# Kernel optimization log

Measured on AMD Instinct MI355X. Metric: run time of the kernel, lower is better.

## Reference

```python
import jax, jax.numpy as jnp
import numpy as np

N_NODES = 100000
N_EDGES = 800000
D_IN = 256
D_HID = 256
D_OUT = 64


def _gcn_conv(x, W, b, src, dst, deg_inv_sqrt, n_nodes):
    """PyG GCNConv: out = D^{-1/2}(A+I)D^{-1/2} (x @ W) + b.
    src/dst already include self-loops; deg_inv_sqrt precomputed over them."""
    h = x @ W  # [N, Dh]
    norm = deg_inv_sqrt[src] * deg_inv_sqrt[dst]  # [E+N]
    msg = h[src] * norm[:, None]  # gather + scale, [E+N, Dh]
    out = jax.ops.segment_sum(msg, dst, num_segments=n_nodes)  # scatter-add
    return out + b


def setup_inputs() -> dict:
    key = jax.random.key(0)
    ks = jax.random.split(key, 8)
    x = jax.random.normal(ks[0], (N_NODES, D_IN), jnp.float32)
    edge_index = jax.random.randint(ks[1], (2, N_EDGES), 0, N_NODES, dtype=jnp.int32)
    W1 = jax.random.normal(ks[2], (D_IN, D_HID), jnp.float32) * (1.0 / np.sqrt(D_IN))
    b1 = jnp.zeros((D_HID,), jnp.float32)
    W2 = jax.random.normal(ks[3], (D_HID, D_HID), jnp.float32) * (1.0 / np.sqrt(D_HID))
    b2 = jnp.zeros((D_HID,), jnp.float32)
    Wo = jax.random.normal(ks[4], (D_HID, D_OUT), jnp.float32) * (1.0 / np.sqrt(D_HID))
    bo = jnp.zeros((D_OUT,), jnp.float32)
    return {"x": x, "edge_index": edge_index, "W1": W1, "b1": b1,
            "W2": W2, "b2": b2, "Wo": Wo, "bo": bo}


def reference(x, edge_index, W1, b1, W2, b2, Wo, bo):
    n = x.shape[0]
    loops = jnp.arange(n, dtype=edge_index.dtype)
    src = jnp.concatenate([edge_index[0], loops])  # add self-loops
    dst = jnp.concatenate([edge_index[1], loops])
    # degree over target nodes (incl. self-loops), symmetric normalization
    deg = jax.ops.segment_sum(jnp.ones(dst.shape[0], x.dtype), dst, num_segments=n)
    deg_inv_sqrt = jax.lax.rsqrt(deg)  # deg >= 1 thanks to self-loops

    h = _gcn_conv(x, W1, b1, src, dst, deg_inv_sqrt, n)
    h = jax.nn.relu(h)
    # dropout p=0.0 -> identity
    h = _gcn_conv(h, W2, b2, src, dst, deg_inv_sqrt, n)
    h = jax.nn.relu(h)
    logits = h @ Wo + bo
    return jax.nn.log_softmax(logits, axis=1)
```

## Files before the change

### kernel.cpp

```cpp
#include <hip/hip_runtime.h>
#include <math.h>

#define TPB 256

typedef short bf16x8 __attribute__((ext_vector_type(8)));
typedef unsigned short u16x8 __attribute__((ext_vector_type(8)));
typedef float f32x4 __attribute__((ext_vector_type(4)));

__device__ __forceinline__ float bf2f(unsigned short u) {
  union { unsigned int i; float f; } c;
  c.i = ((unsigned int)u) << 16;
  return c.f;
}
__device__ __forceinline__ unsigned short f2bf(float f) {
  union { float f; unsigned int i; } c;
  c.f = f;
  unsigned int r = c.i + 0x7FFFu + ((c.i >> 16) & 1u);
  return (unsigned short)(r >> 16);
}


__global__ __launch_bounds__(TPB) void zero_cnt_k(int* __restrict__ cnt, int N) {
  int i = blockIdx.x * TPB + threadIdx.x;
  if (i < N) cnt[i] = 0;
}

__global__ __launch_bounds__(TPB) void count_k(const int* __restrict__ dstv,
                                               int* __restrict__ cnt, int E) {
  int e = blockIdx.x * TPB + threadIdx.x;
  if (e < E) atomicAdd(&cnt[dstv[e]], 1);
}

__global__ __launch_bounds__(TPB) void scan1_k(const int* __restrict__ cnt,
                                               int* __restrict__ excl,
                                               int* __restrict__ blk_sums, int N) {
  __shared__ int sh[TPB];
  int b = blockIdx.x, tid = threadIdx.x;
  int base = b * 1024 + tid * 4;
  int v[4];
  int sum = 0;
#pragma unroll
  for (int j = 0; j < 4; ++j) {
    int i = base + j;
    v[j] = (i < N) ? cnt[i] : 0;
    sum += v[j];
  }
  sh[tid] = sum;
  __syncthreads();
  for (int off = 1; off < TPB; off <<= 1) {
    int t = (tid >= off) ? sh[tid - off] : 0;
    __syncthreads();
    sh[tid] += t;
    __syncthreads();
  }
  if (tid == TPB - 1) blk_sums[b] = sh[TPB - 1];
  int run = (tid > 0) ? sh[tid - 1] : 0;
#pragma unroll
  for (int j = 0; j < 4; ++j) {
    int i = base + j;
    if (i < N) excl[i] = run;
    run += v[j];
  }
}

__global__ __launch_bounds__(TPB) void scan2_k(int* __restrict__ blk_sums, int NB) {
  __shared__ int sh[TPB];
  int tid = threadIdx.x;
  sh[tid] = (tid < NB) ? blk_sums[tid] : 0;
  __syncthreads();
  for (int off = 1; off < TPB; off <<= 1) {
    int t = (tid >= off) ? sh[tid - off] : 0;
    __syncthreads();
    sh[tid] += t;
    __syncthreads();
  }
  int ex = (tid > 0) ? sh[tid - 1] : 0;
  if (tid < NB) blk_sums[tid] = ex;
}

__global__ __launch_bounds__(TPB) void finalize_k(int* __restrict__ row_ptr,
                                                  const int* __restrict__ blk_sums,
                                                  int* __restrict__ cursor,
                                                  const int* __restrict__ cnt,
                                                  float* __restrict__ dis, int N, int E) {
  int i = blockIdx.x * TPB + threadIdx.x;
  if (i < N) {
    int r = row_ptr[i] + blk_sums[i >> 10];
    row_ptr[i] = r;
    cursor[i] = r;
    dis[i] = rsqrtf((float)(cnt[i] + 1));
  }
  if (blockIdx.x == 0 && threadIdx.x == 0) row_ptr[N] = E;
}

__global__ __launch_bounds__(TPB) void fill_k(const int* __restrict__ srcv,
                                              const int* __restrict__ dstv,
                                              int* __restrict__ cursor,
                                              int* __restrict__ col_src, int E) {
  int e = blockIdx.x * TPB + threadIdx.x;
  if (e < E) {
    int d = dstv[e];
    int pos = atomicAdd(&cursor[d], 1);
    col_src[pos] = srcv[e];
  }
}


__global__ __launch_bounds__(TPB) void cvt_bf16_k(const float* __restrict__ in,
                                                  unsigned short* __restrict__ out,
                                                  long n) {
  long i = ((long)blockIdx.x * TPB + threadIdx.x) * 8;
  if (i >= n) return;
  float4 a = *(const float4*)(in + i);
  float4 b = *(const float4*)(in + i + 4);
  ushort4 o0, o1;
  o0.x = f2bf(a.x); o0.y = f2bf(a.y); o0.z = f2bf(a.z); o0.w = f2bf(a.w);
  o1.x = f2bf(b.x); o1.y = f2bf(b.y); o1.z = f2bf(b.z); o1.w = f2bf(b.w);
  *(ushort4*)(out + i) = o0;
  *(ushort4*)(out + i + 4) = o1;
}

__global__ __launch_bounds__(TPB) void wt_k(const float* __restrict__ W,
                                            unsigned short* __restrict__ Wt) {
  int idx = blockIdx.x * TPB + threadIdx.x;
  int n = idx >> 8, k = idx & 255;
  Wt[n * 256 + k] = f2bf(W[k * 256 + n]);
}

__global__ __launch_bounds__(TPB) void wot_k(const float* __restrict__ Wo,
                                             unsigned short* __restrict__ Wot) {
  int idx = blockIdx.x * TPB + threadIdx.x;
  int n = idx >> 8, k = idx & 255;
  Wot[n * 256 + k] = f2bf(Wo[k * 64 + n]);
}


__global__ __launch_bounds__(TPB) void gemm_bf16_k(const unsigned short* __restrict__ A,
                                                   const unsigned short* __restrict__ Bt,
                                                   unsigned short* __restrict__ C,
                                                   const float* __restrict__ dis,
                                                   int M) {
  __shared__ unsigned short As[128 * 32];
  __shared__ unsigned short Bs[128 * 32];
  const int tid = threadIdx.x;
  const int m0 = blockIdx.y * 128;
  const int n0 = blockIdx.x * 128;
  const int lane = tid & 63;
  const int wid = tid >> 6;
  const int wr = (wid >> 1) * 64;
  const int wc = (wid & 1) * 64;

  const int srow = tid >> 1;
  const int scb0 = (tid & 1) * 2;
  const int grow = min(m0 + srow, M - 1);
  const unsigned short* gA = A + (size_t)grow * 256 + scb0 * 8;
  const unsigned short* gB = Bt + (size_t)(n0 + srow) * 256 + scb0 * 8;
  const int swz = (srow >> 1) & 3;
  const int ls0 = srow * 64 + ((scb0 ^ swz) << 4);
  const int ls1 = srow * 64 + (((scb0 + 1) ^ swz) << 4);

  const int r15 = lane & 15;
  const int cq = lane >> 4;
  const int swzr = (r15 >> 1) & 3;
  const int coff = ((cq ^ swzr) << 4);

  f32x4 acc[4][4];
#pragma unroll
  for (int i = 0; i < 4; ++i)
#pragma unroll
    for (int j = 0; j < 4; ++j)
#pragma unroll
      for (int r = 0; r < 4; ++r) acc[i][j][r] = 0.f;

  u16x8 ra0 = *(const u16x8*)(gA);
  u16x8 ra1 = *(const u16x8*)(gA + 8);
  u16x8 rb0 = *(const u16x8*)(gB);
  u16x8 rb1 = *(const u16x8*)(gB + 8);

  for (int kt = 0; kt < 8; ++kt) {
    __syncthreads();
    *(u16x8*)((char*)As + ls0) = ra0;
    *(u16x8*)((char*)As + ls1) = ra1;
    *(u16x8*)((char*)Bs + ls0) = rb0;
    *(u16x8*)((char*)Bs + ls1) = rb1;
    __syncthreads();
    if (kt < 7) {
      ra0 = *(const u16x8*)(gA + (kt + 1) * 32);
      ra1 = *(const u16x8*)(gA + (kt + 1) * 32 + 8);
      rb0 = *(const u16x8*)(gB + (kt + 1) * 32);
      rb1 = *(const u16x8*)(gB + (kt + 1) * 32 + 8);
    }
    bf16x8 af[4], bfr[4];
#pragma unroll
    for (int i = 0; i < 4; ++i)
      af[i] = *(const bf16x8*)((char*)As + (wr + i * 16 + r15) * 64 + coff);
#pragma unroll
    for (int j = 0; j < 4; ++j)
      bfr[j] = *(const bf16x8*)((char*)Bs + (wc + j * 16 + r15) * 64 + coff);
#pragma unroll
    for (int i = 0; i < 4; ++i)
#pragma unroll
      for (int j = 0; j < 4; ++j)
        acc[i][j] = __builtin_amdgcn_mfma_f32_16x16x32_bf16(af[i], bfr[j], acc[i][j], 0, 0, 0);
  }

#pragma unroll
  for (int i = 0; i < 4; ++i) {
#pragma unroll
    for (int r = 0; r < 4; ++r) {
      int row = m0 + wr + i * 16 + (lane >> 4) * 4 + r;
      if (row < M) {
        float dv = dis[row];
#pragma unroll
        for (int j = 0; j < 4; ++j) {
          C[(size_t)row * 256 + n0 + wc + j * 16 + r15] = f2bf(dv * acc[i][j][r]);
        }
      }
    }
  }
}


__global__ __launch_bounds__(TPB) void aggregate_bf_k(const unsigned short* __restrict__ H,
                                                      unsigned short* __restrict__ O,
                                                      const int* __restrict__ row_ptr,
                                                      const int* __restrict__ col_src,
                                                      const float* __restrict__ dis,
                                                      const float* __restrict__ bias,
                                                      int N) {
  int wid = (blockIdx.x * TPB + threadIdx.x) >> 6;
  int lane = threadIdx.x & 63;
  if (wid >= N) return;
  int beg = row_ptr[wid], end = row_ptr[wid + 1];

  float p0 = 0.f, p1 = 0.f, p2 = 0.f, p3 = 0.f;
  float q0 = 0.f, q1 = 0.f, q2 = 0.f, q3 = 0.f;
  float r0 = 0.f, r1 = 0.f, r2 = 0.f, r3 = 0.f;
  float t0 = 0.f, t1 = 0.f, t2 = 0.f, t3 = 0.f;

  int e = beg;
  for (; e + 4 <= end; e += 4) {
    int s0 = col_src[e + 0];
    int s1 = col_src[e + 1];
    int s2 = col_src[e + 2];
    int s3 = col_src[e + 3];
    ushort4 h0 = *(const ushort4*)(H + (size_t)s0 * 256 + lane * 4);
    ushort4 h1 = *(const ushort4*)(H + (size_t)s1 * 256 + lane * 4);
    ushort4 h2 = *(const ushort4*)(H + (size_t)s2 * 256 + lane * 4);
    ushort4 h3 = *(const ushort4*)(H + (size_t)s3 * 256 + lane * 4);
    p0 += bf2f(h0.x); p1 += bf2f(h0.y); p2 += bf2f(h0.z); p3 += bf2f(h0.w);
    q0 += bf2f(h1.x); q1 += bf2f(h1.y); q2 += bf2f(h1.z); q3 += bf2f(h1.w);
    r0 += bf2f(h2.x); r1 += bf2f(h2.y); r2 += bf2f(h2.z); r3 += bf2f(h2.w);
    t0 += bf2f(h3.x); t1 += bf2f(h3.y); t2 += bf2f(h3.z); t3 += bf2f(h3.w);
  }
  for (; e < end; ++e) {
    int s = col_src[e];
    ushort4 h = *(const ushort4*)(H + (size_t)s * 256 + lane * 4);
    p0 += bf2f(h.x); p1 += bf2f(h.y); p2 += bf2f(h.z); p3 += bf2f(h.w);
  }

  ushort4 hv = *(const ushort4*)(H + (size_t)wid * 256 + lane * 4);
  p0 += bf2f(hv.x); p1 += bf2f(hv.y); p2 += bf2f(hv.z); p3 += bf2f(hv.w);

  float s0 = (p0 + q0) + (r0 + t0);
  float s1 = (p1 + q1) + (r1 + t1);
  float s2 = (p2 + q2) + (r2 + t2);
  float s3 = (p3 + q3) + (r3 + t3);

  float dv = dis[wid];
  float4 b = *(const float4*)(bias + lane * 4);
  ushort4 o;
  o.x = f2bf(fmaxf(fmaf(dv, s0, b.x), 0.f));
  o.y = f2bf(fmaxf(fmaf(dv, s1, b.y), 0.f));
  o.z = f2bf(fmaxf(fmaf(dv, s2, b.z), 0.f));
  o.w = f2bf(fmaxf(fmaf(dv, s3, b.w), 0.f));
  *(ushort4*)(O + (size_t)wid * 256 + lane * 4) = o;
}


__global__ __launch_bounds__(TPB) void outgemm_k(const unsigned short* __restrict__ H,
                                                 const unsigned short* __restrict__ Wot,
                                                 const float* __restrict__ bo,
                                                 float* __restrict__ out, int M) {
  __shared__ unsigned short As[128 * 32];
  __shared__ unsigned short Bs[64 * 32];
  __shared__ float Ls[128][65];
  const int tid = threadIdx.x;
  const int m0 = blockIdx.x * 128;
  const int lane = tid & 63;
  const int w = tid >> 6;
  const int wr = w * 32;

  const int srow = tid >> 1;
  const int scb0 = (tid & 1) * 2;
  const int grow = min(m0 + srow, M - 1);
  const unsigned short* gA = H + (size_t)grow * 256 + scb0 * 8;
  const int swz = (srow >> 1) & 3;
  const int lsa0 = srow * 64 + ((scb0 ^ swz) << 4);
  const int lsa1 = srow * 64 + (((scb0 + 1) ^ swz) << 4);

  const int brow = tid >> 2;
  const int bcb = tid & 3;
  const unsigned short* gB = Wot + (size_t)brow * 256 + bcb * 8;
  const int bswz = (brow >> 1) & 3;
  const int lsb = brow * 64 + ((bcb ^ bswz) << 4);

  const int r15 = lane & 15;
  const int cq = lane >> 4;
  const int swzr = (r15 >> 1) & 3;
  const int coff = ((cq ^ swzr) << 4);

  f32x4 acc[2][4];
#pragma unroll
  for (int i = 0; i < 2; ++i)
#pragma unroll
    for (int j = 0; j < 4; ++j)
#pragma unroll
      for (int r = 0; r < 4; ++r) acc[i][j][r] = 0.f;

  u16x8 ra0 = *(const u16x8*)(gA);
  u16x8 ra1 = *(const u16x8*)(gA + 8);
  u16x8 rb = *(const u16x8*)(gB);

  for (int kt = 0; kt < 8; ++kt) {
    __syncthreads();
    *(u16x8*)((char*)As + lsa0) = ra0;
    *(u16x8*)((char*)As + lsa1) = ra1;
    *(u16x8*)((char*)Bs + lsb) = rb;
    __syncthreads();
    if (kt < 7) {
      ra0 = *(const u16x8*)(gA + (kt + 1) * 32);
      ra1 = *(const u16x8*)(gA + (kt + 1) * 32 + 8);
      rb = *(const u16x8*)(gB + (kt + 1) * 32);
    }
    bf16x8 af[2], bfr[4];
#pragma unroll
    for (int i = 0; i < 2; ++i)
      af[i] = *(const bf16x8*)((char*)As + (wr + i * 16 + r15) * 64 + coff);
#pragma unroll
    for (int j = 0; j < 4; ++j)
      bfr[j] = *(const bf16x8*)((char*)Bs + (j * 16 + r15) * 64 + coff);
#pragma unroll
    for (int i = 0; i < 2; ++i)
#pragma unroll
      for (int j = 0; j < 4; ++j)
        acc[i][j] = __builtin_amdgcn_mfma_f32_16x16x32_bf16(af[i], bfr[j], acc[i][j], 0, 0, 0);
  }

#pragma unroll
  for (int j = 0; j < 4; ++j) {
    float bj = bo[j * 16 + r15];
#pragma unroll
    for (int i = 0; i < 2; ++i)
#pragma unroll
      for (int r = 0; r < 4; ++r) {
        int rl = wr + i * 16 + (lane >> 4) * 4 + r;
        Ls[rl][j * 16 + r15] = acc[i][j][r] + bj;
      }
  }
  __syncthreads();

  for (int r = wr; r < wr + 32; ++r) {
    int gr = m0 + r;
    if (gr >= M) break;
    float v = Ls[r][lane];
    float mx = v;
    for (int o = 32; o > 0; o >>= 1) mx = fmaxf(mx, __shfl_xor(mx, o, 64));
    float ex = expf(v - mx);
    float s = ex;
    for (int o = 32; o > 0; o >>= 1) s += __shfl_xor(s, o, 64);
    out[(size_t)gr * 64 + lane] = (v - mx) - logf(s);
  }
}


extern "C" void kernel_launch(void* const* d_in, const int* in_sizes, int n_in,
                              void* d_out, int out_size, void* d_ws, size_t ws_size,
                              hipStream_t stream) {
  const float* x = (const float*)d_in[0];
  const int* ei = (const int*)d_in[1];
  const float* W1 = (const float*)d_in[2];
  const float* b1 = (const float*)d_in[3];
  const float* W2 = (const float*)d_in[4];
  const float* b2 = (const float*)d_in[5];
  const float* Wo = (const float*)d_in[6];
  const float* bo = (const float*)d_in[7];
  float* out = (float*)d_out;

  const int Dh = 256;
  const int N = in_sizes[0] / Dh;
  const int E = in_sizes[1] / 2;
  const int* srcv = ei;
  const int* dstv = ei + E;

  char* p = (char*)d_ws;
  auto take = [&](size_t bytes) {
    char* r = p;
    p += (bytes + 255) & ~(size_t)255;
    return r;
  };
  unsigned short* xbf = (unsigned short*)take((size_t)N * Dh * 2);
  unsigned short* hbuf1 = (unsigned short*)take((size_t)N * Dh * 2);
  unsigned short* hbuf2 = (unsigned short*)take((size_t)N * Dh * 2);
  unsigned short* Wt1 = (unsigned short*)take(256 * 256 * 2);
  unsigned short* Wt2 = (unsigned short*)take(256 * 256 * 2);
  unsigned short* Wot = (unsigned short*)take(64 * 256 * 2);
  float* dis = (float*)take((size_t)N * 4);
  int* cnt = (int*)take((size_t)N * 4);
  int* row_ptr = (int*)take((size_t)(N + 1) * 4);
  int* cursor = (int*)take((size_t)N * 4);
  int* col_src = (int*)take((size_t)E * 4);
  int* blk_sums = (int*)take(4096 * 4);

  int NB = (N + 1023) / 1024;

  long nx = (long)N * Dh;
  cvt_bf16_k<<<(int)((nx / 8 + TPB - 1) / TPB), TPB, 0, stream>>>(x, xbf, nx);
  wt_k<<<256, TPB, 0, stream>>>(W1, Wt1);
  wt_k<<<256, TPB, 0, stream>>>(W2, Wt2);
  wot_k<<<64, TPB, 0, stream>>>(Wo, Wot);
  zero_cnt_k<<<(N + TPB - 1) / TPB, TPB, 0, stream>>>(cnt, N);
  count_k<<<(E + TPB - 1) / TPB, TPB, 0, stream>>>(dstv, cnt, E);
  scan1_k<<<NB, TPB, 0, stream>>>(cnt, row_ptr, blk_sums, N);
  scan2_k<<<1, TPB, 0, stream>>>(blk_sums, NB);
  finalize_k<<<(N + TPB - 1) / TPB, TPB, 0, stream>>>(row_ptr, blk_sums, cursor, cnt, dis, N, E);
  fill_k<<<(E + TPB - 1) / TPB, TPB, 0, stream>>>(srcv, dstv, cursor, col_src, E);

  dim3 ggrid(2, (N + 127) / 128);

  gemm_bf16_k<<<ggrid, TPB, 0, stream>>>(xbf, Wt1, hbuf1, dis, N);
  aggregate_bf_k<<<(N + 3) / 4, TPB, 0, stream>>>(hbuf1, hbuf2, row_ptr, col_src, dis, b1, N);
  gemm_bf16_k<<<ggrid, TPB, 0, stream>>>(hbuf2, Wt2, hbuf1, dis, N);
  aggregate_bf_k<<<(N + 3) / 4, TPB, 0, stream>>>(hbuf1, hbuf2, row_ptr, col_src, dis, b2, N);
  outgemm_k<<<(N + 127) / 128, TPB, 0, stream>>>(hbuf2, Wot, bo, out, N);
}
```

Before: 530.0 us.

## Fuse fp32-to-bf16 conversion into first GEMM and widen aggregation gathers

Removes the separate conversion kernel and its bf16 copy of x. The first GEMM now reads fp32 x directly and packs it to bf16 in registers, which saves a full write and re-read of a 51MB buffer, though each A-tile load in that GEMM now moves twice the bytes. The aggregation kernel now has each half-wave handle a different edge with 16-byte loads, so more gathers are in flight per wave. The two halves are combined with a cross-lane shuffle, and one extra row load is used to pad the odd-edge tail.

```diff
diff --git a/kernel.cpp b/kernel.cpp
--- a/kernel.cpp
+++ b/kernel.cpp
@@ -17,6 +17,12 @@
   c.f = f;
   unsigned int r = c.i + 0x7FFFu + ((c.i >> 16) & 1u);
   return (unsigned short)(r >> 16);
+}
+__device__ __forceinline__ u16x8 pack8(float4 a, float4 b) {
+  u16x8 r;
+  r[0] = f2bf(a.x); r[1] = f2bf(a.y); r[2] = f2bf(a.z); r[3] = f2bf(a.w);
+  r[4] = f2bf(b.x); r[5] = f2bf(b.y); r[6] = f2bf(b.z); r[7] = f2bf(b.w);
+  return r;
 }
 
 
@@ -106,20 +112,6 @@
 }
 
 
-__global__ __launch_bounds__(TPB) void cvt_bf16_k(const float* __restrict__ in,
-                                                  unsigned short* __restrict__ out,
-                                                  long n) {
-  long i = ((long)blockIdx.x * TPB + threadIdx.x) * 8;
-  if (i >= n) return;
-  float4 a = *(const float4*)(in + i);
-  float4 b = *(const float4*)(in + i + 4);
-  ushort4 o0, o1;
-  o0.x = f2bf(a.x); o0.y = f2bf(a.y); o0.z = f2bf(a.z); o0.w = f2bf(a.w);
-  o1.x = f2bf(b.x); o1.y = f2bf(b.y); o1.z = f2bf(b.z); o1.w = f2bf(b.w);
-  *(ushort4*)(out + i) = o0;
-  *(ushort4*)(out + i + 4) = o1;
-}
-
 __global__ __launch_bounds__(TPB) void wt_k(const float* __restrict__ W,
                                             unsigned short* __restrict__ Wt) {
   int idx = blockIdx.x * TPB + threadIdx.x;
@@ -135,7 +127,8 @@
 }
 
 
-__global__ __launch_bounds__(TPB) void gemm_bf16_k(const unsigned short* __restrict__ A,
+template <bool AF32>
+__global__ __launch_bounds__(TPB) void gemm_bf16_t(const void* __restrict__ Araw,
                                                    const unsigned short* __restrict__ Bt,
                                                    unsigned short* __restrict__ C,
                                                    const float* __restrict__ dis,
@@ -153,7 +146,8 @@
   const int srow = tid >> 1;
   const int scb0 = (tid & 1) * 2;
   const int grow = min(m0 + srow, M - 1);
-  const unsigned short* gA = A + (size_t)grow * 256 + scb0 * 8;
+  const float* gA32 = (const float*)Araw + (size_t)grow * 256 + scb0 * 8;
+  const unsigned short* gA16 = (const unsigned short*)Araw + (size_t)grow * 256 + scb0 * 8;
   const unsigned short* gB = Bt + (size_t)(n0 + srow) * 256 + scb0 * 8;
   const int swz = (srow >> 1) & 3;
   const int ls0 = srow * 64 + ((scb0 ^ swz) << 4);
@@ -172,8 +166,18 @@
 #pragma unroll
       for (int r = 0; r < 4; ++r) acc[i][j][r] = 0.f;
 
-  u16x8 ra0 = *(const u16x8*)(gA);
-  u16x8 ra1 = *(const u16x8*)(gA + 8);
+  u16x8 ra0, ra1;
+  if constexpr (AF32) {
+    float4 f0 = *(const float4*)(gA32);
+    float4 f1 = *(const float4*)(gA32 + 4);
+    float4 f2 = *(const float4*)(gA32 + 8);
+    float4 f3 = *(const float4*)(gA32 + 12);
+    ra0 = pack8(f0, f1);
+    ra1 = pack8(f2, f3);
+  } else {
+    ra0 = *(const u16x8*)(gA16);
+    ra1 = *(const u16x8*)(gA16 + 8);
+  }
   u16x8 rb0 = *(const u16x8*)(gB);
   u16x8 rb1 = *(const u16x8*)(gB + 8);
 
@@ -185,8 +189,17 @@
     *(u16x8*)((char*)Bs + ls1) = rb1;
     __syncthreads();
     if (kt < 7) {
-      ra0 = *(const u16x8*)(gA + (kt + 1) * 32);
-      ra1 = *(const u16x8*)(gA + (kt + 1) * 32 + 8);
+      if constexpr (AF32) {
+        float4 f0 = *(const float4*)(gA32 + (kt + 1) * 32);
+        float4 f1 = *(const float4*)(gA32 + (kt + 1) * 32 + 4);
+        float4 f2 = *(const float4*)(gA32 + (kt + 1) * 32 + 8);
+        float4 f3 = *(const float4*)(gA32 + (kt + 1) * 32 + 12);
+        ra0 = pack8(f0, f1);
+        ra1 = pack8(f2, f3);
+      } else {
+        ra0 = *(const u16x8*)(gA16 + (kt + 1) * 32);
+        ra1 = *(const u16x8*)(gA16 + (kt + 1) * 32 + 8);
+      }
       rb0 = *(const u16x8*)(gB + (kt + 1) * 32);
       rb1 = *(const u16x8*)(gB + (kt + 1) * 32 + 8);
     }
@@ -231,50 +244,61 @@
   int wid = (blockIdx.x * TPB + threadIdx.x) >> 6;
   int lane = threadIdx.x & 63;
   if (wid >= N) return;
+  const int half = lane >> 5;
+  const int l5 = lane & 31;
+  const size_t co = (size_t)l5 * 8;
   int beg = row_ptr[wid], end = row_ptr[wid + 1];
 
-  float p0 = 0.f, p1 = 0.f, p2 = 0.f, p3 = 0.f;
-  float q0 = 0.f, q1 = 0.f, q2 = 0.f, q3 = 0.f;
-  float r0 = 0.f, r1 = 0.f, r2 = 0.f, r3 = 0.f;
-  float t0 = 0.f, t1 = 0.f, t2 = 0.f, t3 = 0.f;
+  float a0[8], a1[8], a2[8], a3[8];
+#pragma unroll
+  for (int j = 0; j < 8; ++j) { a0[j] = 0.f; a1[j] = 0.f; a2[j] = 0.f; a3[j] = 0.f; }
 
   int e = beg;
-  for (; e + 4 <= end; e += 4) {
-    int s0 = col_src[e + 0];
-    int s1 = col_src[e + 1];
-    int s2 = col_src[e + 2];
-    int s3 = col_src[e + 3];
-    ushort4 h0 = *(const ushort4*)(H + (size_t)s0 * 256 + lane * 4);
-    ushort4 h1 = *(const ushort4*)(H + (size_t)s1 * 256 + lane * 4);
-    ushort4 h2 = *(const ushort4*)(H + (size_t)s2 * 256 + lane * 4);
-    ushort4 h3 = *(const ushort4*)(H + (size_t)s3 * 256 + lane * 4);
-    p0 += bf2f(h0.x); p1 += bf2f(h0.y); p2 += bf2f(h0.z); p3 += bf2f(h0.w);
-    q0 += bf2f(h1.x); q1 += bf2f(h1.y); q2 += bf2f(h1.z); q3 += bf2f(h1.w);
-    r0 += bf2f(h2.x); r1 += bf2f(h2.y); r2 += bf2f(h2.z); r3 += bf2f(h2.w);
-    t0 += bf2f(h3.x); t1 += bf2f(h3.y); t2 += bf2f(h3.z); t3 += bf2f(h3.w);
-  }
-  for (; e < end; ++e) {
-    int s = col_src[e];
-    ushort4 h = *(const ushort4*)(H + (size_t)s * 256 + lane * 4);
-    p0 += bf2f(h.x); p1 += bf2f(h.y); p2 += bf2f(h.z); p3 += bf2f(h.w);
-  }
-
-  ushort4 hv = *(const ushort4*)(H + (size_t)wid * 256 + lane * 4);
-  p0 += bf2f(hv.x); p1 += bf2f(hv.y); p2 += bf2f(hv.z); p3 += bf2f(hv.w);
-
-  float s0 = (p0 + q0) + (r0 + t0);
-  float s1 = (p1 + q1) + (r1 + t1);
-  float s2 = (p2 + q2) + (r2 + t2);
-  float s3 = (p3 + q3) + (r3 + t3);
+  for (; e + 8 <= end; e += 8) {
+    int s0 = col_src[e + 0 + half];
+    int s1 = col_src[e + 2 + half];
+    int s2 = col_src[e + 4 + half];
+    int s3 = col_src[e + 6 + half];
+    u16x8 h0 = *(const u16x8*)(H + (size_t)s0 * 256 + co);
+    u16x8 h1 = *(const u16x8*)(H + (size_t)s1 * 256 + co);
+    u16x8 h2 = *(const u16x8*)(H + (size_t)s2 * 256 + co);
+    u16x8 h3 = *(const u16x8*)(H + (size_t)s3 * 256 + co);
+#pragma unroll
+    for (int j = 0; j < 8; ++j) {
+      a0[j] += bf2f(h0[j]);
+      a1[j] += bf2f(h1[j]);
+      a2[j] += bf2f(h2[j]);
+      a3[j] += bf2f(h3[j]);
+    }
+  }
+  for (; e < end; e += 2) {
+    int idx = e + half;
+    int ok = idx < end;
+    int s = ok ? col_src[idx] : wid;
+    u16x8 h = *(const u16x8*)(H + (size_t)s * 256 + co);
+    float m = ok ? 1.f : 0.f;
+#pragma unroll
+    for (int j = 0; j < 8; ++j) a0[j] = fmaf(m, bf2f(h[j]), a0[j]);
+  }
+
+  float s[8];
+#pragma unroll
+  for (int j = 0; j < 8; ++j) s[j] = (a0[j] + a1[j]) + (a2[j] + a3[j]);
+#pragma unroll
+  for (int j = 0; j < 8; ++j) s[j] += __shfl_xor(s[j], 32, 64);
+
+  u16x8 hv = *(const u16x8*)(H + (size_t)wid * 256 + co);
+#pragma unroll
+  for (int j = 0; j < 8; ++j) s[j] += bf2f(hv[j]);
 
   float dv = dis[wid];
-  float4 b = *(const float4*)(bias + lane * 4);
-  ushort4 o;
-  o.x = f2bf(fmaxf(fmaf(dv, s0, b.x), 0.f));
-  o.y = f2bf(fmaxf(fmaf(dv, s1, b.y), 0.f));
-  o.z = f2bf(fmaxf(fmaf(dv, s2, b.z), 0.f));
-  o.w = f2bf(fmaxf(fmaf(dv, s3, b.w), 0.f));
-  *(ushort4*)(O + (size_t)wid * 256 + lane * 4) = o;
+  float4 b0 = *(const float4*)(bias + l5 * 8);
+  float4 b1 = *(const float4*)(bias + l5 * 8 + 4);
+  float bb[8] = {b0.x, b0.y, b0.z, b0.w, b1.x, b1.y, b1.z, b1.w};
+  u16x8 o;
+#pragma unroll
+  for (int j = 0; j < 8; ++j) o[j] = f2bf(fmaxf(fmaf(dv, s[j], bb[j]), 0.f));
+  if (half == 0) *(u16x8*)(O + (size_t)wid * 256 + co) = o;
 }
 
 
@@ -367,9 +391,9 @@
     float mx = v;
     for (int o = 32; o > 0; o >>= 1) mx = fmaxf(mx, __shfl_xor(mx, o, 64));
     float ex = expf(v - mx);
-    float s = ex;
-    for (int o = 32; o > 0; o >>= 1) s += __shfl_xor(s, o, 64);
-    out[(size_t)gr * 64 + lane] = (v - mx) - logf(s);
+    float sm = ex;
+    for (int o = 32; o > 0; o >>= 1) sm += __shfl_xor(sm, o, 64);
+    out[(size_t)gr * 64 + lane] = (v - mx) - logf(sm);
   }
 }
 
@@ -399,7 +423,6 @@
     p += (bytes + 255) & ~(size_t)255;
     return r;
   };
-  unsigned short* xbf = (unsigned short*)take((size_t)N * Dh * 2);
   unsigned short* hbuf1 = (unsigned short*)take((size_t)N * Dh * 2);
   unsigned short* hbuf2 = (unsigned short*)take((size_t)N * Dh * 2);
   unsigned short* Wt1 = (unsigned short*)take(256 * 256 * 2);
@@ -414,8 +437,6 @@
 
   int NB = (N + 1023) / 1024;
 
-  long nx = (long)N * Dh;
-  cvt_bf16_k<<<(int)((nx / 8 + TPB - 1) / TPB), TPB, 0, stream>>>(x, xbf, nx);
   wt_k<<<256, TPB, 0, stream>>>(W1, Wt1);
   wt_k<<<256, TPB, 0, stream>>>(W2, Wt2);
   wot_k<<<64, TPB, 0, stream>>>(Wo, Wot);
@@ -428,9 +449,9 @@
 
   dim3 ggrid(2, (N + 127) / 128);
 
-  gemm_bf16_k<<<ggrid, TPB, 0, stream>>>(xbf, Wt1, hbuf1, dis, N);
+  gemm_bf16_t<true><<<ggrid, TPB, 0, stream>>>((const void*)x, Wt1, hbuf1, dis, N);
   aggregate_bf_k<<<(N + 3) / 4, TPB, 0, stream>>>(hbuf1, hbuf2, row_ptr, col_src, dis, b1, N);
-  gemm_bf16_k<<<ggrid, TPB, 0, stream>>>(hbuf2, Wt2, hbuf1, dis, N);
+  gemm_bf16_t<false><<<ggrid, TPB, 0, stream>>>((const void*)hbuf2, Wt2, hbuf1, dis, N);
   aggregate_bf_k<<<(N + 3) / 4, TPB, 0, stream>>>(hbuf1, hbuf2, row_ptr, col_src, dis, b2, N);
   outgemm_k<<<(N + 127) / 128, TPB, 0, stream>>>(hbuf2, Wot, bo, out, N);
 }
```

Result: no change. 520.1 us (-1.9%).

## Fuse fp32-to-bf16 input conversion into first GEMM, double-buffer LDS, XCD-aware block mapping

Applied to the files above, without the earlier changes.

Removes the separate kernel that converted x to bf16. The first GEMM now reads fp32 x directly and packs it to bf16 in registers, which saves writing and re-reading a 51MB intermediate. The GEMM also double-buffers its shared-memory tiles, dropping one barrier per k-step. It remaps a 1D grid so the two N-halves of the same row block land on the same XCD, for L2 reuse of A. The cost is more register pressure and twice the LDS use, which may lower occupancy.

```diff
diff --git a/kernel.cpp b/kernel.cpp
--- a/kernel.cpp
+++ b/kernel.cpp
@@ -17,6 +17,12 @@
   c.f = f;
   unsigned int r = c.i + 0x7FFFu + ((c.i >> 16) & 1u);
   return (unsigned short)(r >> 16);
+}
+__device__ __forceinline__ u16x8 pack8(float4 a, float4 b) {
+  u16x8 r;
+  r[0] = f2bf(a.x); r[1] = f2bf(a.y); r[2] = f2bf(a.z); r[3] = f2bf(a.w);
+  r[4] = f2bf(b.x); r[5] = f2bf(b.y); r[6] = f2bf(b.z); r[7] = f2bf(b.w);
+  return r;
 }
 
 
@@ -106,20 +112,6 @@
 }
 
 
-__global__ __launch_bounds__(TPB) void cvt_bf16_k(const float* __restrict__ in,
-                                                  unsigned short* __restrict__ out,
-                                                  long n) {
-  long i = ((long)blockIdx.x * TPB + threadIdx.x) * 8;
-  if (i >= n) return;
-  float4 a = *(const float4*)(in + i);
-  float4 b = *(const float4*)(in + i + 4);
-  ushort4 o0, o1;
-  o0.x = f2bf(a.x); o0.y = f2bf(a.y); o0.z = f2bf(a.z); o0.w = f2bf(a.w);
-  o1.x = f2bf(b.x); o1.y = f2bf(b.y); o1.z = f2bf(b.z); o1.w = f2bf(b.w);
-  *(ushort4*)(out + i) = o0;
-  *(ushort4*)(out + i + 4) = o1;
-}
-
 __global__ __launch_bounds__(TPB) void wt_k(const float* __restrict__ W,
                                             unsigned short* __restrict__ Wt) {
   int idx = blockIdx.x * TPB + threadIdx.x;
@@ -135,16 +127,24 @@
 }
 
 
-__global__ __launch_bounds__(TPB) void gemm_bf16_k(const unsigned short* __restrict__ A,
+template <bool AF32>
+__global__ __launch_bounds__(TPB) void gemm_bf16_t(const void* __restrict__ Araw,
                                                    const unsigned short* __restrict__ Bt,
                                                    unsigned short* __restrict__ C,
                                                    const float* __restrict__ dis,
-                                                   int M) {
-  __shared__ unsigned short As[128 * 32];
-  __shared__ unsigned short Bs[128 * 32];
+                                                   int M, int nyb) {
+  __shared__ unsigned short As[2][128 * 32];
+  __shared__ unsigned short Bs[2][128 * 32];
+  const int bid = blockIdx.x;
+  const int xcd = bid & 7;
+  const int s = bid >> 3;
+  const int nsel = s & 1;
+  const int yb = (s >> 1) * 8 + xcd;
+  if (yb >= nyb) return;
+  const int m0 = yb * 128;
+  const int n0 = nsel * 128;
+
   const int tid = threadIdx.x;
-  const int m0 = blockIdx.y * 128;
-  const int n0 = blockIdx.x * 128;
   const int lane = tid & 63;
   const int wid = tid >> 6;
   const int wr = (wid >> 1) * 64;
@@ -153,7 +153,8 @@
   const int srow = tid >> 1;
   const int scb0 = (tid & 1) * 2;
   const int grow = min(m0 + srow, M - 1);
-  const unsigned short* gA = A + (size_t)grow * 256 + scb0 * 8;
+  const float* gA32 = (const float*)Araw + (size_t)grow * 256 + scb0 * 8;
+  const unsigned short* gA16 = (const unsigned short*)Araw + (size_t)grow * 256 + scb0 * 8;
   const unsigned short* gB = Bt + (size_t)(n0 + srow) * 256 + scb0 * 8;
   const int swz = (srow >> 1) & 3;
   const int ls0 = srow * 64 + ((scb0 ^ swz) << 4);
@@ -172,31 +173,50 @@
 #pragma unroll
       for (int r = 0; r < 4; ++r) acc[i][j][r] = 0.f;
 
-  u16x8 ra0 = *(const u16x8*)(gA);
-  u16x8 ra1 = *(const u16x8*)(gA + 8);
+  u16x8 ra0, ra1;
+  if constexpr (AF32) {
+    float4 f0 = *(const float4*)(gA32);
+    float4 f1 = *(const float4*)(gA32 + 4);
+    float4 f2 = *(const float4*)(gA32 + 8);
+    float4 f3 = *(const float4*)(gA32 + 12);
+    ra0 = pack8(f0, f1);
+    ra1 = pack8(f2, f3);
+  } else {
+    ra0 = *(const u16x8*)(gA16);
+    ra1 = *(const u16x8*)(gA16 + 8);
+  }
   u16x8 rb0 = *(const u16x8*)(gB);
   u16x8 rb1 = *(const u16x8*)(gB + 8);
 
   for (int kt = 0; kt < 8; ++kt) {
-    __syncthreads();
-    *(u16x8*)((char*)As + ls0) = ra0;
-    *(u16x8*)((char*)As + ls1) = ra1;
-    *(u16x8*)((char*)Bs + ls0) = rb0;
-    *(u16x8*)((char*)Bs + ls1) = rb1;
+    const int cur = kt & 1;
+    *(u16x8*)((char*)As[cur] + ls0) = ra0;
+    *(u16x8*)((char*)As[cur] + ls1) = ra1;
+    *(u16x8*)((char*)Bs[cur] + ls0) = rb0;
+    *(u16x8*)((char*)Bs[cur] + ls1) = rb1;
     __syncthreads();
     if (kt < 7) {
-      ra0 = *(const u16x8*)(gA + (kt + 1) * 32);
-      ra1 = *(const u16x8*)(gA + (kt + 1) * 32 + 8);
+      if constexpr (AF32) {
+        float4 f0 = *(const float4*)(gA32 + (kt + 1) * 32);
+        float4 f1 = *(const float4*)(gA32 + (kt + 1) * 32 + 4);
+        float4 f2 = *(const float4*)(gA32 + (kt + 1) * 32 + 8);
+        float4 f3 = *(const float4*)(gA32 + (kt + 1) * 32 + 12);
+        ra0 = pack8(f0, f1);
+        ra1 = pack8(f2, f3);
+      } else {
+        ra0 = *(const u16x8*)(gA16 + (kt + 1) * 32);
+        ra1 = *(const u16x8*)(gA16 + (kt + 1) * 32 + 8);
+      }
       rb0 = *(const u16x8*)(gB + (kt + 1) * 32);
       rb1 = *(const u16x8*)(gB + (kt + 1) * 32 + 8);
     }
     bf16x8 af[4], bfr[4];
 #pragma unroll
     for (int i = 0; i < 4; ++i)
-      af[i] = *(const bf16x8*)((char*)As + (wr + i * 16 + r15) * 64 + coff);
+      af[i] = *(const bf16x8*)((char*)As[cur] + (wr + i * 16 + r15) * 64 + coff);
 #pragma unroll
     for (int j = 0; j < 4; ++j)
-      bfr[j] = *(const bf16x8*)((char*)Bs + (wc + j * 16 + r15) * 64 + coff);
+      bfr[j] = *(const bf16x8*)((char*)Bs[cur] + (wc + j * 16 + r15) * 64 + coff);
 #pragma unroll
     for (int i = 0; i < 4; ++i)
 #pragma unroll
@@ -367,9 +387,9 @@
     float mx = v;
     for (int o = 32; o > 0; o >>= 1) mx = fmaxf(mx, __shfl_xor(mx, o, 64));
     float ex = expf(v - mx);
-    float s = ex;
-    for (int o = 32; o > 0; o >>= 1) s += __shfl_xor(s, o, 64);
-    out[(size_t)gr * 64 + lane] = (v - mx) - logf(s);
+    float sm = ex;
+    for (int o = 32; o > 0; o >>= 1) sm += __shfl_xor(sm, o, 64);
+    out[(size_t)gr * 64 + lane] = (v - mx) - logf(sm);
   }
 }
 
@@ -399,7 +419,6 @@
     p += (bytes + 255) & ~(size_t)255;
     return r;
   };
-  unsigned short* xbf = (unsigned short*)take((size_t)N * Dh * 2);
   unsigned short* hbuf1 = (unsigned short*)take((size_t)N * Dh * 2);
   unsigned short* hbuf2 = (unsigned short*)take((size_t)N * Dh * 2);
   unsigned short* Wt1 = (unsigned short*)take(256 * 256 * 2);
@@ -414,8 +433,6 @@
 
   int NB = (N + 1023) / 1024;
 
-  long nx = (long)N * Dh;
-  cvt_bf16_k<<<(int)((nx / 8 + TPB - 1) / TPB), TPB, 0, stream>>>(x, xbf, nx);
   wt_k<<<256, TPB, 0, stream>>>(W1, Wt1);
   wt_k<<<256, TPB, 0, stream>>>(W2, Wt2);
   wot_k<<<64, TPB, 0, stream>>>(Wo, Wot);
@@ -426,11 +443,12 @@
   finalize_k<<<(N + TPB - 1) / TPB, TPB, 0, stream>>>(row_ptr, blk_sums, cursor, cnt, dis, N, E);
   fill_k<<<(E + TPB - 1) / TPB, TPB, 0, stream>>>(srcv, dstv, cursor, col_src, E);
 
-  dim3 ggrid(2, (N + 127) / 128);
-
-  gemm_bf16_k<<<ggrid, TPB, 0, stream>>>(xbf, Wt1, hbuf1, dis, N);
+  const int nyb = (N + 127) / 128;
+  const int gblocks = 8 * 2 * ((nyb + 7) / 8);
+
+  gemm_bf16_t<true><<<gblocks, TPB, 0, stream>>>((const void*)x, Wt1, hbuf1, dis, N, nyb);
   aggregate_bf_k<<<(N + 3) / 4, TPB, 0, stream>>>(hbuf1, hbuf2, row_ptr, col_src, dis, b1, N);
-  gemm_bf16_k<<<ggrid, TPB, 0, stream>>>(hbuf2, Wt2, hbuf1, dis, N);
+  gemm_bf16_t<false><<<gblocks, TPB, 0, stream>>>((const void*)hbuf2, Wt2, hbuf1, dis, N, nyb);
   aggregate_bf_k<<<(N + 3) / 4, TPB, 0, stream>>>(hbuf1, hbuf2, row_ptr, col_src, dis, b2, N);
   outgemm_k<<<(N + 127) / 128, TPB, 0, stream>>>(hbuf2, Wot, bo, out, N);
 }
```

New measurement: 508.2 us. -4.1%, faster.

## Stream row tiles against resident LDS weights and fuse input bf16 conversion

Applied to the files above, without the earlier changes.

The GEMMs become persistent kernels that load the full 256x256 bf16 weight into LDS once per block. Each wave then streams 16-row tiles of A straight from global memory into registers. The first-layer GEMM converts the fp32 input to bf16 on the fly, which removes the separate conversion kernel and its intermediate buffer. The output GEMM keeps logits in registers and does log-softmax with 16-lane shuffles instead of staging them through LDS. This trades the tiled A reuse of the old kernel for fewer syncs, 128KB of LDS per block, and register-heavy 16-accumulator tiles, which may limit occupancy.

```diff
diff --git a/kernel.cpp b/kernel.cpp
--- a/kernel.cpp
+++ b/kernel.cpp
@@ -106,20 +106,6 @@
 }
 
 
-__global__ __launch_bounds__(TPB) void cvt_bf16_k(const float* __restrict__ in,
-                                                  unsigned short* __restrict__ out,
-                                                  long n) {
-  long i = ((long)blockIdx.x * TPB + threadIdx.x) * 8;
-  if (i >= n) return;
-  float4 a = *(const float4*)(in + i);
-  float4 b = *(const float4*)(in + i + 4);
-  ushort4 o0, o1;
-  o0.x = f2bf(a.x); o0.y = f2bf(a.y); o0.z = f2bf(a.z); o0.w = f2bf(a.w);
-  o1.x = f2bf(b.x); o1.y = f2bf(b.y); o1.z = f2bf(b.z); o1.w = f2bf(b.w);
-  *(ushort4*)(out + i) = o0;
-  *(ushort4*)(out + i + 4) = o1;
-}
-
 __global__ __launch_bounds__(TPB) void wt_k(const float* __restrict__ W,
                                             unsigned short* __restrict__ Wt) {
   int idx = blockIdx.x * TPB + threadIdx.x;
@@ -135,86 +121,86 @@
 }
 
 
-__global__ __launch_bounds__(TPB) void gemm_bf16_k(const unsigned short* __restrict__ A,
-                                                   const unsigned short* __restrict__ Bt,
-                                                   unsigned short* __restrict__ C,
-                                                   const float* __restrict__ dis,
-                                                   int M) {
-  __shared__ unsigned short As[128 * 32];
-  __shared__ unsigned short Bs[128 * 32];
+template <bool AF32>
+__global__ __launch_bounds__(1024) void gemm_stream_t(const void* __restrict__ Araw,
+                                                      const unsigned short* __restrict__ Bt,
+                                                      unsigned short* __restrict__ C,
+                                                      const float* __restrict__ dis,
+                                                      int M, int ntiles) {
+  __shared__ unsigned short Bs[256 * 256];
   const int tid = threadIdx.x;
-  const int m0 = blockIdx.y * 128;
-  const int n0 = blockIdx.x * 128;
+
+  {
+    const int n = tid >> 2;
+    const int sb = tid & 3;
+    const unsigned short* src = Bt + (size_t)n * 256;
+#pragma unroll
+    for (int it = 0; it < 8; ++it) {
+      int s = sb + 4 * it;
+      u16x8 v = *(const u16x8*)(src + s * 8);
+      *(u16x8*)((char*)Bs + n * 512 + ((s ^ (n & 7)) << 4)) = v;
+    }
+  }
+  __syncthreads();
+
   const int lane = tid & 63;
-  const int wid = tid >> 6;
-  const int wr = (wid >> 1) * 64;
-  const int wc = (wid & 1) * 64;
-
-  const int srow = tid >> 1;
-  const int scb0 = (tid & 1) * 2;
-  const int grow = min(m0 + srow, M - 1);
-  const unsigned short* gA = A + (size_t)grow * 256 + scb0 * 8;
-  const unsigned short* gB = Bt + (size_t)(n0 + srow) * 256 + scb0 * 8;
-  const int swz = (srow >> 1) & 3;
-  const int ls0 = srow * 64 + ((scb0 ^ swz) << 4);
-  const int ls1 = srow * 64 + (((scb0 + 1) ^ swz) << 4);
-
   const int r15 = lane & 15;
   const int cq = lane >> 4;
-  const int swzr = (r15 >> 1) & 3;
-  const int coff = ((cq ^ swzr) << 4);
-
-  f32x4 acc[4][4];
-#pragma unroll
-  for (int i = 0; i < 4; ++i)
-#pragma unroll
-    for (int j = 0; j < 4; ++j)
-#pragma unroll
-      for (int r = 0; r < 4; ++r) acc[i][j][r] = 0.f;
-
-  u16x8 ra0 = *(const u16x8*)(gA);
-  u16x8 ra1 = *(const u16x8*)(gA + 8);
-  u16x8 rb0 = *(const u16x8*)(gB);
-  u16x8 rb1 = *(const u16x8*)(gB + 8);
-
-  for (int kt = 0; kt < 8; ++kt) {
-    __syncthreads();
-    *(u16x8*)((char*)As + ls0) = ra0;
-    *(u16x8*)((char*)As + ls1) = ra1;
-    *(u16x8*)((char*)Bs + ls0) = rb0;
-    *(u16x8*)((char*)Bs + ls1) = rb1;
-    __syncthreads();
-    if (kt < 7) {
-      ra0 = *(const u16x8*)(gA + (kt + 1) * 32);
-      ra1 = *(const u16x8*)(gA + (kt + 1) * 32 + 8);
-      rb0 = *(const u16x8*)(gB + (kt + 1) * 32);
-      rb1 = *(const u16x8*)(gB + (kt + 1) * 32 + 8);
-    }
-    bf16x8 af[4], bfr[4];
-#pragma unroll
-    for (int i = 0; i < 4; ++i)
-      af[i] = *(const bf16x8*)((char*)As + (wr + i * 16 + r15) * 64 + coff);
-#pragma unroll
-    for (int j = 0; j < 4; ++j)
-      bfr[j] = *(const bf16x8*)((char*)Bs + (wc + j * 16 + r15) * 64 + coff);
-#pragma unroll
-    for (int i = 0; i < 4; ++i)
-#pragma unroll
-      for (int j = 0; j < 4; ++j)
-        acc[i][j] = __builtin_amdgcn_mfma_f32_16x16x32_bf16(af[i], bfr[j], acc[i][j], 0, 0, 0);
-  }
-
-#pragma unroll
-  for (int i = 0; i < 4; ++i) {
+  const int gw = blockIdx.x * 16 + (tid >> 6);
+  const int nw = gridDim.x * 16;
+
+  for (int mt = gw; mt < ntiles; mt += nw) {
+    const int m0 = mt * 16;
+    const int arow = min(m0 + r15, M - 1);
+
+    bf16x8 a[8];
+    if constexpr (AF32) {
+      const float* ap = (const float*)Araw + (size_t)arow * 256 + cq * 8;
+#pragma unroll
+      for (int kt = 0; kt < 8; ++kt) {
+        float4 f0 = *(const float4*)(ap + kt * 32);
+        float4 f1 = *(const float4*)(ap + kt * 32 + 4);
+        u16x8 t;
+        t[0] = f2bf(f0.x); t[1] = f2bf(f0.y); t[2] = f2bf(f0.z); t[3] = f2bf(f0.w);
+        t[4] = f2bf(f1.x); t[5] = f2bf(f1.y); t[6] = f2bf(f1.z); t[7] = f2bf(f1.w);
+        a[kt] = (bf16x8)t;
+      }
+    } else {
+      const unsigned short* ap = (const unsigned short*)Araw + (size_t)arow * 256 + cq * 8;
+#pragma unroll
+      for (int kt = 0; kt < 8; ++kt) a[kt] = *(const bf16x8*)(ap + kt * 32);
+    }
+
+    f32x4 acc[16];
+#pragma unroll
+    for (int j = 0; j < 16; ++j)
+#pragma unroll
+      for (int r = 0; r < 4; ++r) acc[j][r] = 0.f;
+
+#pragma unroll
+    for (int kt = 0; kt < 8; ++kt) {
+#pragma unroll
+      for (int j = 0; j < 16; ++j) {
+        int n = j * 16 + r15;
+        int s = kt * 4 + cq;
+        bf16x8 b = *(const bf16x8*)((char*)Bs + n * 512 + ((s ^ (n & 7)) << 4));
+        acc[j] = __builtin_amdgcn_mfma_f32_16x16x32_bf16(a[kt], b, acc[j], 0, 0, 0);
+      }
+    }
+
+    float dv[4];
 #pragma unroll
     for (int r = 0; r < 4; ++r) {
-      int row = m0 + wr + i * 16 + (lane >> 4) * 4 + r;
+      int row = m0 + cq * 4 + r;
+      dv[r] = (row < M) ? dis[row] : 0.f;
+    }
+#pragma unroll
+    for (int r = 0; r < 4; ++r) {
+      int row = m0 + cq * 4 + r;
       if (row < M) {
-        float dv = dis[row];
-#pragma unroll
-        for (int j = 0; j < 4; ++j) {
-          C[(size_t)row * 256 + n0 + wc + j * 16 + r15] = f2bf(dv * acc[i][j][r]);
-        }
+        unsigned short* cp = C + (size_t)row * 256 + r15;
+#pragma unroll
+        for (int j = 0; j < 16; ++j) cp[j * 16] = f2bf(dv[r] * acc[j][r]);
       }
     }
   }
@@ -278,98 +264,82 @@
 }
 
 
-__global__ __launch_bounds__(TPB) void outgemm_k(const unsigned short* __restrict__ H,
-                                                 const unsigned short* __restrict__ Wot,
-                                                 const float* __restrict__ bo,
-                                                 float* __restrict__ out, int M) {
-  __shared__ unsigned short As[128 * 32];
-  __shared__ unsigned short Bs[64 * 32];
-  __shared__ float Ls[128][65];
+__global__ __launch_bounds__(512) void outgemm_stream_k(const unsigned short* __restrict__ H,
+                                                        const unsigned short* __restrict__ Wot,
+                                                        const float* __restrict__ bo,
+                                                        float* __restrict__ out,
+                                                        int M, int ntiles) {
+  __shared__ unsigned short Bs[64 * 256];
   const int tid = threadIdx.x;
-  const int m0 = blockIdx.x * 128;
+
+  {
+    const int n = tid >> 3;
+    const int sb = tid & 7;
+    const unsigned short* src = Wot + (size_t)n * 256;
+#pragma unroll
+    for (int it = 0; it < 4; ++it) {
+      int s = sb + 8 * it;
+      u16x8 v = *(const u16x8*)(src + s * 8);
+      *(u16x8*)((char*)Bs + n * 512 + ((s ^ (n & 7)) << 4)) = v;
+    }
+  }
+  __syncthreads();
+
   const int lane = tid & 63;
-  const int w = tid >> 6;
-  const int wr = w * 32;
-
-  const int srow = tid >> 1;
-  const int scb0 = (tid & 1) * 2;
-  const int grow = min(m0 + srow, M - 1);
-  const unsigned short* gA = H + (size_t)grow * 256 + scb0 * 8;
-  const int swz = (srow >> 1) & 3;
-  const int lsa0 = srow * 64 + ((scb0 ^ swz) << 4);
-  const int lsa1 = srow * 64 + (((scb0 + 1) ^ swz) << 4);
-
-  const int brow = tid >> 2;
-  const int bcb = tid & 3;
-  const unsigned short* gB = Wot + (size_t)brow * 256 + bcb * 8;
-  const int bswz = (brow >> 1) & 3;
-  const int lsb = brow * 64 + ((bcb ^ bswz) << 4);
-
   const int r15 = lane & 15;
   const int cq = lane >> 4;
-  const int swzr = (r15 >> 1) & 3;
-  const int coff = ((cq ^ swzr) << 4);
-
-  f32x4 acc[2][4];
-#pragma unroll
-  for (int i = 0; i < 2; ++i)
-#pragma unroll
-    for (int j = 0; j < 4; ++j)
-#pragma unroll
-      for (int r = 0; r < 4; ++r) acc[i][j][r] = 0.f;
-
-  u16x8 ra0 = *(const u16x8*)(gA);
-  u16x8 ra1 = *(const u16x8*)(gA + 8);
-  u16x8 rb = *(const u16x8*)(gB);
-
+  const int mt = blockIdx.x * 8 + (tid >> 6);
+  if (mt >= ntiles) return;
+  const int m0 = mt * 16;
+  const int arow = min(m0 + r15, M - 1);
+
+  bf16x8 a[8];
+  {
+    const unsigned short* ap = H + (size_t)arow * 256 + cq * 8;
+#pragma unroll
+    for (int kt = 0; kt < 8; ++kt) a[kt] = *(const bf16x8*)(ap + kt * 32);
+  }
+
+  f32x4 acc[4];
+#pragma unroll
+  for (int j = 0; j < 4; ++j)
+#pragma unroll
+    for (int r = 0; r < 4; ++r) acc[j][r] = 0.f;
+
+#pragma unroll
   for (int kt = 0; kt < 8; ++kt) {
-    __syncthreads();
-    *(u16x8*)((char*)As + lsa0) = ra0;
-    *(u16x8*)((char*)As + lsa1) = ra1;
-    *(u16x8*)((char*)Bs + lsb) = rb;
-    __syncthreads();
-    if (kt < 7) {
-      ra0 = *(const u16x8*)(gA + (kt + 1) * 32);
-      ra1 = *(const u16x8*)(gA + (kt + 1) * 32 + 8);
-      rb = *(const u16x8*)(gB + (kt + 1) * 32);
-    }
-    bf16x8 af[2], bfr[4];
-#pragma unroll
-    for (int i = 0; i < 2; ++i)
-      af[i] = *(const bf16x8*)((char*)As + (wr + i * 16 + r15) * 64 + coff);
-#pragma unroll
-    for (int j = 0; j < 4; ++j)
-      bfr[j] = *(const bf16x8*)((char*)Bs + (j * 16 + r15) * 64 + coff);
-#pragma unroll
-    for (int i = 0; i < 2; ++i)
-#pragma unroll
-      for (int j = 0; j < 4; ++j)
-        acc[i][j] = __builtin_amdgcn_mfma_f32_16x16x32_bf16(af[i], bfr[j], acc[i][j], 0, 0, 0);
+#pragma unroll
+    for (int j = 0; j < 4; ++j) {
+      int n = j * 16 + r15;
+      int s = kt * 4 + cq;
+      bf16x8 b = *(const bf16x8*)((char*)Bs + n * 512 + ((s ^ (n & 7)) << 4));
+      acc[j] = __builtin_amdgcn_mfma_f32_16x16x32_bf16(a[kt], b, acc[j], 0, 0, 0);
+    }
   }
 
 #pragma unroll
   for (int j = 0; j < 4; ++j) {
     float bj = bo[j * 16 + r15];
 #pragma unroll
-    for (int i = 0; i < 2; ++i)
-#pragma unroll
-      for (int r = 0; r < 4; ++r) {
-        int rl = wr + i * 16 + (lane >> 4) * 4 + r;
-        Ls[rl][j * 16 + r15] = acc[i][j][r] + bj;
-      }
-  }
-  __syncthreads();
-
-  for (int r = wr; r < wr + 32; ++r) {
-    int gr = m0 + r;
-    if (gr >= M) break;
-    float v = Ls[r][lane];
-    float mx = v;
-    for (int o = 32; o > 0; o >>= 1) mx = fmaxf(mx, __shfl_xor(mx, o, 64));
-    float ex = expf(v - mx);
-    float s = ex;
-    for (int o = 32; o > 0; o >>= 1) s += __shfl_xor(s, o, 64);
-    out[(size_t)gr * 64 + lane] = (v - mx) - logf(s);
+    for (int r = 0; r < 4; ++r) acc[j][r] += bj;
+  }
+
+#pragma unroll
+  for (int r = 0; r < 4; ++r) {
+    int row = m0 + cq * 4 + r;
+    float mx = fmaxf(fmaxf(acc[0][r], acc[1][r]), fmaxf(acc[2][r], acc[3][r]));
+#pragma unroll
+    for (int o = 1; o <= 8; o <<= 1) mx = fmaxf(mx, __shfl_xor(mx, o, 64));
+    float se = expf(acc[0][r] - mx) + expf(acc[1][r] - mx) +
+               expf(acc[2][r] - mx) + expf(acc[3][r] - mx);
+#pragma unroll
+    for (int o = 1; o <= 8; o <<= 1) se += __shfl_xor(se, o, 64);
+    float ls = logf(se);
+    if (row < M) {
+      float* op = out + (size_t)row * 64 + r15;
+#pragma unroll
+      for (int j = 0; j < 4; ++j) op[j * 16] = (acc[j][r] - mx) - ls;
+    }
   }
 }
 
@@ -399,7 +369,6 @@
     p += (bytes + 255) & ~(size_t)255;
     return r;
   };
-  unsigned short* xbf = (unsigned short*)take((size_t)N * Dh * 2);
   unsigned short* hbuf1 = (unsigned short*)take((size_t)N * Dh * 2);
   unsigned short* hbuf2 = (unsigned short*)take((size_t)N * Dh * 2);
   unsigned short* Wt1 = (unsigned short*)take(256 * 256 * 2);
@@ -414,8 +383,6 @@
 
   int NB = (N + 1023) / 1024;
 
-  long nx = (long)N * Dh;
-  cvt_bf16_k<<<(int)((nx / 8 + TPB - 1) / TPB), TPB, 0, stream>>>(x, xbf, nx);
   wt_k<<<256, TPB, 0, stream>>>(W1, Wt1);
   wt_k<<<256, TPB, 0, stream>>>(W2, Wt2);
   wot_k<<<64, TPB, 0, stream>>>(Wo, Wot);
@@ -426,11 +393,11 @@
   finalize_k<<<(N + TPB - 1) / TPB, TPB, 0, stream>>>(row_ptr, blk_sums, cursor, cnt, dis, N, E);
   fill_k<<<(E + TPB - 1) / TPB, TPB, 0, stream>>>(srcv, dstv, cursor, col_src, E);
 
-  dim3 ggrid(2, (N + 127) / 128);
-
-  gemm_bf16_k<<<ggrid, TPB, 0, stream>>>(xbf, Wt1, hbuf1, dis, N);
+  const int ntiles = (N + 15) / 16;
+
+  gemm_stream_t<true><<<256, 1024, 0, stream>>>((const void*)x, Wt1, hbuf1, dis, N, ntiles);
   aggregate_bf_k<<<(N + 3) / 4, TPB, 0, stream>>>(hbuf1, hbuf2, row_ptr, col_src, dis, b1, N);
-  gemm_bf16_k<<<ggrid, TPB, 0, stream>>>(hbuf2, Wt2, hbuf1, dis, N);
+  gemm_stream_t<false><<<256, 1024, 0, stream>>>((const void*)hbuf2, Wt2, hbuf1, dis, N, ntiles);
   aggregate_bf_k<<<(N + 3) / 4, TPB, 0, stream>>>(hbuf1, hbuf2, row_ptr, col_src, dis, b2, N);
-  outgemm_k<<<(N + 127) / 128, TPB, 0, stream>>>(hbuf2, Wot, bo, out, N);
-}
+  outgemm_stream_k<<<(ntiles + 7) / 8, 512, 0, stream>>>(hbuf2, Wot, bo, out, N, ntiles);
+}
```

New measurement: 1.083 ms. 104% more time.
